# Kernel tuning notes

Hardware: AMD Instinct MI355X
Metric: run time of the kernel (lower is better)

## Reference

```python
import jax, jax.numpy as jnp
import numpy as np
from jax import lax

MAX_LEN = 50
MIN_LEN = 5
S = 2 * MAX_LEN + 1  # 101 states (2 branches)
NEG = -10000.0       # score for disallowed transitions


def _build_constraints():
    """Replicates CRFBaseModel.get_crf_constraints(max_len=50, min_len=5, n_branches=2)."""
    pairs = [(0, 0), (0, 1), (MAX_LEN, 1), (MAX_LEN, 0)]
    for i in range(1, MAX_LEN):
        pairs.append((i, i + 1))
        if i > MIN_LEN - 1:
            pairs.append((MIN_LEN - 2, i))
    pairs.append((MAX_LEN - 1, MAX_LEN))
    pairs.append((MAX_LEN - 1, MAX_LEN - 1))
    start_b = 1 + MAX_LEN
    end_b = 2 * MAX_LEN
    pairs += [(0, start_b), (end_b, start_b), (end_b, 0), (end_b, 1), (start_b - 1, start_b)]
    for i in range(start_b, end_b):
        pairs.append((i, i + 1))
        if i > MIN_LEN - 1:
            pairs.append((start_b + MIN_LEN - 3, i))
    pairs.append((end_b - 1, end_b - 1))
    allowed_t = np.zeros((S, S), dtype=bool)
    for (a, c) in pairs:
        allowed_t[a, c] = True
    allowed_s = np.zeros((S,), dtype=bool)
    allowed_s[[0, 1, start_b]] = True
    allowed_e = np.zeros((S,), dtype=bool)
    allowed_e[[0, MAX_LEN, end_b]] = True
    return allowed_t, allowed_s, allowed_e

_ALLOWED_T, _ALLOWED_S, _ALLOWED_E = _build_constraints()


def setup_inputs() -> dict:
    key = jax.random.key(0)
    k0, k1, k2, k3, k4 = jax.random.split(key, 5)
    B, T = 128, 2048
    features = jax.random.normal(k0, (B, T, 64), dtype=jnp.float32)
    mask = jnp.ones((B, T), dtype=bool)
    W = jax.random.normal(k1, (64, 3), dtype=jnp.float32) * 0.05
    b = jnp.zeros((3,), dtype=jnp.float32)
    start_transitions = jax.random.uniform(k2, (S,), minval=-0.1, maxval=0.1, dtype=jnp.float32)
    transitions = jax.random.uniform(k3, (S, S), minval=-0.1, maxval=0.1, dtype=jnp.float32)
    end_transitions = jax.random.uniform(k4, (S,), minval=-0.1, maxval=0.1, dtype=jnp.float32)
    return {"features": features, "mask": mask, "W": W, "b": b,
            "start_transitions": start_transitions, "transitions": transitions,
            "end_transitions": end_transitions}


def reference(features, mask, W, b, start_transitions, transitions, end_transitions):
    B, T, _ = features.shape
    # Apply hand-crafted transition constraints (disallowed -> -10000).
    trans = jnp.where(jnp.asarray(_ALLOWED_T), transitions, NEG)       # [S,S]
    start = jnp.where(jnp.asarray(_ALLOWED_S), start_transitions, NEG)  # [S]
    end = jnp.where(jnp.asarray(_ALLOWED_E), end_transitions, NEG)      # [S]

    # Emissions: linear head to 3 labels, repeated over the state space.
    e3 = features @ W + b  # [B,T,3]
    em = jnp.concatenate([
        e3[..., 0:1],
        jnp.broadcast_to(e3[..., 1:2], (B, T, MAX_LEN)),
        jnp.broadcast_to(e3[..., 2:3], (B, T, MAX_LEN)),
    ], axis=-1)  # [B,T,S]

    eT = jnp.moveaxis(em, 1, 0)    # [T,B,S]
    mT = jnp.moveaxis(mask, 1, 0)  # [T,B]

    # ---- forward (alpha) recursion ----
    a0 = start[None, :] + eT[0]  # [B,S]

    def fwd_step(a, inp):
        e_t, m_t = inp
        a_new = jax.nn.logsumexp(a[:, :, None] + trans[None], axis=1) + e_t
        a = jnp.where(m_t[:, None], a_new, a)
        return a, a

    _, alphas = lax.scan(fwd_step, a0, (eT[1:], mT[1:]))
    alpha = jnp.concatenate([a0[None], alphas], axis=0)  # [T,B,S]
    logZ = jax.nn.logsumexp(alpha[-1] + end[None, :], axis=-1)  # [B]

    # ---- backward (beta) recursion ----
    bT = jnp.broadcast_to(end[None, :], (B, S))

    def bwd_step(b_nxt, inp):
        e_nxt, m_nxt = inp
        b_new = jax.nn.logsumexp(trans[None] + (e_nxt + b_nxt)[:, None, :], axis=2)
        b_nxt = jnp.where(m_nxt[:, None], b_new, b_nxt)
        return b_nxt, b_nxt

    _, betas = lax.scan(bwd_step, bT, (eT[1:], mT[1:]), reverse=True)
    beta = jnp.concatenate([betas, bT[None]], axis=0)  # [T,B,S]

    # marginal probabilities p_t(s) = exp(alpha+beta-logZ) == softmax over states
    probs = jnp.moveaxis(jax.nn.softmax(alpha + beta, axis=-1), 0, 1)  # [B,T,S]

    # ---- Viterbi decode (top_k=1) ----
    def vit_step(v, inp):
        e_t, m_t = inp
        scores = v[:, :, None] + trans[None]   # [B,S_prev,S_cur]
        best = scores.max(axis=1)
        idx = scores.argmax(axis=1).astype(jnp.int32)
        v = jnp.where(m_t[:, None], best + e_t, v)
        return v, idx

    v_last, hist = lax.scan(vit_step, a0, (eT[1:], mT[1:]))  # hist: [T-1,B,S]
    final = v_last + end[None, :]
    last_state = jnp.argmax(final, axis=-1).astype(jnp.int32)  # [B]
    best_score = final.max(axis=-1)

    def back(state, h_t):
        prev = jnp.take_along_axis(h_t, state[:, None], axis=1)[:, 0]
        return prev, prev

    _, prevs = lax.scan(back, last_state, hist, reverse=True)  # [T-1,B]
    paths = jnp.concatenate([prevs, last_state[None]], axis=0).T  # [B,T]
    path_probs = jnp.exp(best_score - logZ)  # [B]
    return probs, paths, path_probs
```

## Files before the change

kernel.cpp:

```cpp
#include <hip/hip_runtime.h>
#include <hip/hip_bf16.h>
#include <math.h>

#define Tn 2048
#define Bn 128
#define Sn 101
#define HP 112
#define CL 128
#define NC (Tn / CL)
#define SEG 256
#define KSEG 8
#define SEGA 128
#define KA 16
#define WWA 64
#define WWARMV 512
#define NEGV -10000.0f
#define DIS  -3.0e38f
#define NINF2 -1.0e30f
#define L2E  1.442695041f

__device__ __forceinline__ int state_label(int s) { return (s == 0) ? 0 : ((s <= 50) ? 1 : 2); }

__device__ __forceinline__ float rl(float v, int lane) {
    return __int_as_float(__builtin_amdgcn_readlane(__float_as_int(v), lane));
}
__device__ __forceinline__ float slog2(float x) {
    return (x > 0.f) ? __log2f(x) : NINF2;
}

__device__ __forceinline__ float dpp_shr1(float x) {
    int xi = __float_as_int(x);
    return __int_as_float(__builtin_amdgcn_update_dpp(xi, xi, 0x138, 0xf, 0xf, false));
}
__device__ __forceinline__ float dpp_shl1(float x) {
    int xi = __float_as_int(x);
    return __int_as_float(__builtin_amdgcn_update_dpp(xi, xi, 0x130, 0xf, 0xf, false));
}
__device__ __forceinline__ float dpp_sum63(float x) {
    x += __int_as_float(__builtin_amdgcn_update_dpp(0, __float_as_int(x), 0x111, 0xf, 0xf, false));
    x += __int_as_float(__builtin_amdgcn_update_dpp(0, __float_as_int(x), 0x112, 0xf, 0xf, false));
    x += __int_as_float(__builtin_amdgcn_update_dpp(0, __float_as_int(x), 0x114, 0xf, 0xf, false));
    x += __int_as_float(__builtin_amdgcn_update_dpp(0, __float_as_int(x), 0x118, 0xf, 0xf, false));
    x += __int_as_float(__builtin_amdgcn_update_dpp(0, __float_as_int(x), 0x142, 0xf, 0xf, false));
    x += __int_as_float(__builtin_amdgcn_update_dpp(0, __float_as_int(x), 0x143, 0xf, 0xf, false));
    return x;
}
__device__ __forceinline__ float dpp_max63(float x) {
    x = fmaxf(x, __int_as_float(__builtin_amdgcn_update_dpp(0, __float_as_int(x), 0x111, 0xf, 0xf, false)));
    x = fmaxf(x, __int_as_float(__builtin_amdgcn_update_dpp(0, __float_as_int(x), 0x112, 0xf, 0xf, false)));
    x = fmaxf(x, __int_as_float(__builtin_amdgcn_update_dpp(0, __float_as_int(x), 0x114, 0xf, 0xf, false)));
    x = fmaxf(x, __int_as_float(__builtin_amdgcn_update_dpp(0, __float_as_int(x), 0x118, 0xf, 0xf, false)));
    x = fmaxf(x, __int_as_float(__builtin_amdgcn_update_dpp(0, __float_as_int(x), 0x142, 0xf, 0xf, false)));
    x = fmaxf(x, __int_as_float(__builtin_amdgcn_update_dpp(0, __float_as_int(x), 0x143, 0xf, 0xf, false)));
    return x;
}
__device__ __forceinline__ void renorm2(float& a, float& b, float& sh) {
    float m = rl(dpp_max63(fmaxf(a, b)), 63);
    int mi = __float_as_int(m);
    if (mi == 0) return;
    int e = ((mi >> 23) & 255) - 127;
    float sc = __int_as_float((127 - e) << 23);
    a *= sc; b *= sc; sh += (float)e;
}

__device__ __forceinline__ float lse2_tree(float vA, float vB) {
    float m = fmaxf(vA, vB);
    float z = exp2f(vA - m) + exp2f(vB - m);
    #pragma unroll
    for (int o = 32; o; o >>= 1) {
        float mo = __shfl_xor(m, o), zo = __shfl_xor(z, o);
        float mx = fmaxf(m, mo);
        z = z * exp2f(m - mx) + zo * exp2f(mo - mx);
        m = mx;
    }
    return m + __log2f(z);
}

__device__ __forceinline__ void load_panel(const float* __restrict__ e3, size_t ebase, int pb, int l,
                                           float& q0, float& q1, float& q2) {
    int tr = pb + l;
    if (tr > Tn - 1) tr = Tn - 1;
    if (tr < 0) tr = 0;
    const float* p = e3 + (ebase + tr) * 3;
    q0 = p[0]; q1 = p[1]; q2 = p[2];
}
__device__ __forceinline__ void panel_sel2(float q0, float q1, float q2, int u,
                                           int l, float& eA, float& eB) {
    float s0 = rl(q0, u), s1 = rl(q1, u), s2 = rl(q2, u);
    eA = (l == 0) ? s0 : ((l <= 25) ? s1 : s2);
    eB = (l <= 24) ? s1 : s2;
}

__device__ __forceinline__ void bwd_lin(float eA, float eB, float& bA, float& bB,
    float wAc, float wBc, float wAs, float wBs, float wA2, float wA3,
    float w3A, float w3B, float w53A, float w53B, int l)
{
    float yA = eA * bA, yB = eB * bB;
    float yAdn = dpp_shl1(yA);
    float y0 = rl(yA, 0), y1 = rl(yB, 0), y51 = rl(yB, 25);
    float c3 = w3A * yA + w3B * yB;
    float c53 = w53A * yA + w53B * yB;
    float s3 = rl(dpp_sum63(c3), 63);
    float s53 = rl(dpp_sum63(c53), 63);
    float chA = (l == 50) ? y51 : yB;
    float nA = wAc * chA + wAs * yA + wA2 * y0 + wA3 * ((l == 0) ? y51 : y1);
    float nB = wBc * yAdn + wBs * yB;
    nB = (l == 1) ? s3 : ((l == 26) ? s53 : nB);
    bA = nA; bB = nB;
}

__global__ __launch_bounds__(256) void k_emis(const float* __restrict__ feat,
                                              const float* __restrict__ W,
                                              const float* __restrict__ bb,
                                              float* __restrict__ e3) {
    int row = blockIdx.x * 256 + threadIdx.x;
    if (row >= Bn * Tn) return;
    const float* f = feat + (size_t)row * 64;
    double a0 = 0.0, a1 = 0.0, a2 = 0.0;
    for (int i = 0; i < 64; i++) {
        double fv = (double)f[i];
        a0 += fv * (double)W[i * 3 + 0];
        a1 += fv * (double)W[i * 3 + 1];
        a2 += fv * (double)W[i * 3 + 2];
    }
    e3[(size_t)row * 3 + 0] = (float)(a0 + (double)bb[0]);
    e3[(size_t)row * 3 + 1] = (float)(a1 + (double)bb[1]);
    e3[(size_t)row * 3 + 2] = (float)(a2 + (double)bb[2]);
}

__global__ __launch_bounds__(64) void kA(const float* __restrict__ e3,
                                         const float* __restrict__ trans,
                                         const float* __restrict__ startT,
                                         const float* __restrict__ endT,
                                         float* __restrict__ alphaOut,
                                         float* __restrict__ shf,
                                         float* __restrict__ wA,
                                         float* __restrict__ outLast,
                                         float* __restrict__ LSEend,
                                         float* __restrict__ bhand)
{
    const int bid = blockIdx.x;
    const int l = threadIdx.x;
    const int sA = 2 * l, sB = 2 * l + 1;
    const bool hA = sA <= 100, hB = sB <= 100;
    const int lblA = state_label(hA ? sA : 100);
    const int lblB = state_label(hB ? sB : 100);

    if (bid < 2048) {
        const int b = bid >> 4, j = bid & 15;
        const size_t ebase = (size_t)b * Tn;
        const int t0 = j * SEGA, t1 = t0 + SEGA;
        int ts = t0 - WWA; if (ts < 0) ts = 0;
        float trAc = (hA && sA >= 1) ? trans[(sA - 1) * Sn + sA] : DIS;
        float trBc = hB ? trans[(sB - 1) * Sn + sB] : DIS;
        float trA1 = (sA >= 5 && sA <= 49) ? trans[3 * Sn + sA] : ((hA && sA <= 1) ? trans[50 * Sn + sA] : DIS);
        float trB1 = (sB >= 5 && sB <= 49) ? trans[3 * Sn + sB] : ((hB && sB <= 1) ? trans[50 * Sn + sB] : DIS);
        float trA2 = ((sA == 51 || sA == 52) || (sA >= 55 && sA <= 99)) ? trans[53 * Sn + sA]
                   : ((hA && sA <= 1) ? trans[100 * Sn + sA] : DIS);
        float trB2 = ((sB == 51 || sB == 52) || (sB >= 55 && sB <= 99)) ? trans[53 * Sn + sB]
                   : ((hB && sB <= 1) ? trans[100 * Sn + sB] : DIS);
        float trA3 = (sA == 0) ? trans[0] : DIS;
        float trB3 = (sB == 49 || sB == 53 || sB == 99) ? trans[sB * Sn + sB] : ((sB == 51) ? trans[0 * Sn + 51] : DIS);
        float trBx = (sB == 51) ? trans[100 * Sn + 51] : DIS;
        float wAc = __expf(trAc), wB0 = __expf(trBc), wA1 = __expf(trA1), wB1 = __expf(trB1);
        float wA2w = __expf(trA2), wB2 = __expf(trB2), wA3w = __expf(trA3), wB3 = __expf(trB3), wBx = __expf(trBx);
        float scA = (sA == 0 || sA == 1 || sA == 51) ? startT[sA] : NEGV;
        float scB = (sB == 1 || sB == 51) ? startT[sB] : NEGV;
        float enA = (sA == 0 || sA == 50 || sA == 100) ? endT[sA] : NEGV;

        float p0, p1, p2, n0 = 0.f, n1 = 0.f, n2 = 0.f;
        int pb = ts + 1;
        load_panel(e3, ebase, pb, l, p0, p1, p2);
        p0 = __expf(p0); p1 = __expf(p1); p2 = __expf(p2);

        float aA, aB, sh = 0.f;
        if (ts == 0) {
            float e0A = e3[ebase * 3 + lblA], e0B = e3[ebase * 3 + lblB];
            aA = __expf(scA + e0A);
            aB = __expf(scB + e0B);
            if (j == 0) {
                size_t r = ebase * Sn;
                if (hA) alphaOut[r + sA] = aA;
                if (hB) alphaOut[r + sB] = aB;
                if (l == 0) shf[ebase] = 0.f;
            }
        } else { aA = 1.f; aB = 1.f; }
        int rn = 0;
        int tb = ts + 1;
        for (; tb + 8 <= t0; tb += 8) {
            if ((rn++ & 1) == 0) renorm2(aA, aB, sh);
            if (tb - pb >= 64) { p0 = __expf(n0); p1 = __expf(n1); p2 = __expf(n2); pb += 64; }
            if (tb - pb == 48 && pb + 64 < t1) load_panel(e3, ebase, pb + 64, l, n0, n1, n2);
            #pragma unroll
            for (int v = 0; v < 8; ++v) {
                int t = tb + v;
                float eA, eB;
                panel_sel2(p0, p1, p2, t - pb, l, eA, eB);
                float chA = dpp_shr1(aB);
                float h3 = rl(aB, 1), h53 = rl(aB, 26);
                float a0v = rl(aA, 0), a50v = rl(aA, 25), a100v = rl(aA, 50);
                float s1v = (l == 0) ? a50v : h3;
                float s2v = (l == 0) ? a100v : h53;
                float zA = wAc * chA + wA1 * s1v + wA2w * s2v + wA3w * aA;
                float zB = wB0 * aA + wB1 * s1v + wB2 * s2v + wB3 * ((l == 25) ? a0v : aB) + wBx * a100v;
                aA = zA * eA; aB = zB * eB;
            }
        }
        for (; tb < t1; tb += 8) {
            if ((rn++ & 1) == 0) renorm2(aA, aB, sh);
            if (tb - pb >= 64) { p0 = __expf(n0); p1 = __expf(n1); p2 = __expf(n2); pb += 64; }
            if (tb - pb == 48 && pb + 64 < t1) load_panel(e3, ebase, pb + 64, l, n0, n1, n2);
            #pragma unroll
            for (int v = 0; v < 8; ++v) {
                int t = tb + v;
                if (t < t1) {
                    float eA, eB;
                    panel_sel2(p0, p1, p2, t - pb, l, eA, eB);
                    float chA = dpp_shr1(aB);
                    float h3 = rl(aB, 1), h53 = rl(aB, 26);
                    float a0v = rl(aA, 0), a50v = rl(aA, 25), a100v = rl(aA, 50);
                    float s1v = (l == 0) ? a50v : h3;
                    float s2v = (l == 0) ? a100v : h53;
                    float zA = wAc * chA + wA1 * s1v + wA2w * s2v + wA3w * aA;
                    float zB = wB0 * aA + wB1 * s1v + wB2 * s2v + wB3 * ((l == 25) ? a0v : aB) + wBx * a100v;
                    aA = zA * eA; aB = zB * eB;
                    if (t >= t0) {
                        size_t r = (ebase + t) * Sn;
                        if (hA) alphaOut[r + sA] = aA;
                        if (hB) alphaOut[r + sB] = aB;
                        if (l == 0) shf[ebase + t] = sh;
                    }
                    if (t == t0 - 1 && l == 0) wA[b * KA + j] = slog2(aA) + sh;
                }
            }
        }
        if (l == 0) outLast[b * KA + j] = slog2(aA) + sh;
        if (j == KA - 1) {
            float N = lse2_tree(hA ? slog2(aA) + sh + enA * L2E : NINF2,
                                hB ? slog2(aB) + sh + NEGV * L2E : NINF2);
            if (l == 0) LSEend[b] = N;
        }
    } else {
        const int x = bid - 2048;
        const int b = x >> 4, j = x & 15;
        const size_t ebase = (size_t)b * Tn;
        const int tend = j * SEGA + SEGA;
        int te = tend + WWA; if (te > Tn - 1) te = Tn - 1;
        float trAc = (l < 50) ? trans[sA * Sn + sA + 1] : ((l == 50) ? trans[100 * Sn + 51] : DIS);
        float trBc = (hB && l != 1 && l != 26) ? trans[sB * Sn + sB + 1] : DIS;
        float trAs = (sA == 0) ? trans[0] : DIS;
        float trBs = (sB == 49) ? trans[49 * Sn + 49] : ((sB == 99) ? trans[99 * Sn + 99] : DIS);
        float trA2c = (sA == 50) ? trans[50 * Sn + 0] : ((sA == 100) ? trans[100 * Sn + 0] : DIS);
        float trA3c = (sA == 0) ? trans[0 * Sn + 51]
                    : ((sA == 50) ? trans[50 * Sn + 1] : ((sA == 100) ? trans[100 * Sn + 1] : DIS));
        float tr3A = (sA >= 4 && sA <= 49) ? trans[3 * Sn + sA] : DIS;
        float tr3B = (sB >= 4 && sB <= 49) ? trans[3 * Sn + sB] : DIS;
        float tr53A = (sA >= 51 && sA <= 99) ? trans[53 * Sn + sA] : DIS;
        float tr53B = (sB >= 51 && sB <= 99) ? trans[53 * Sn + sB] : DIS;
        float wAc = __expf(trAc), wBc = __expf(trBc), wAs = __expf(trAs), wBs = __expf(trBs);
        float wA2 = __expf(trA2c), wA3 = __expf(trA3c);
        float w3A = __expf(tr3A), w3B = __expf(tr3B), w53A = __expf(tr53A), w53B = __expf(tr53B);
        float bA, bB, sh = 0.f;
        if (te == Tn - 1) {
            bA = (sA == 0 || sA == 50 || sA == 100) ? __expf(endT[sA]) : 0.f;
            bB = 0.f;
        } else { bA = 1.f; bB = 1.f; }
        if (te > tend) {
            float p0, p1, p2, n0 = 0.f, n1 = 0.f, n2 = 0.f;
            int pb = te - 63;
            load_panel(e3, ebase, pb, l, p0, p1, p2);
            p0 = __expf(p0); p1 = __expf(p1); p2 = __expf(p2);
            int rn = 0;
            for (int tc = te; tc > tend; tc -= 8) {
                if ((rn++ & 1) == 0) renorm2(bA, bB, sh);
                if (tc < pb) { p0 = __expf(n0); p1 = __expf(n1); p2 = __expf(n2); pb -= 64; }
                if (tc - pb == 7 && pb - 1 > tend) load_panel(e3, ebase, pb - 64, l, n0, n1, n2);
                #pragma unroll
                for (int v = 0; v < 8; ++v) {
                    int tcur = tc - v;
                    if (tcur > tend) {
                        float eA, eB;
                        panel_sel2(p0, p1, p2, tcur - pb, l, eA, eB);
                        bwd_lin(eA, eB, bA, bB, wAc, wBc, wAs, wBs, wA2, wA3,
                                w3A, w3B, w53A, w53B, l);
                    }
                }
            }
        }
        float* h0 = bhand + (size_t)(b * KA + j) * 104;
        if (l <= 50) { h0[2 * l] = slog2(bA) + sh; h0[2 * l + 1] = slog2(bB) + sh; }
    }
}

__global__ __launch_bounds__(64) void kB(const float* __restrict__ e3,
                                         const float* __restrict__ trans,
                                         const float* __restrict__ startT,
                                         const float* __restrict__ endT,
                                         const float* __restrict__ bhand,
                                         const float* __restrict__ shf,
                                         float* __restrict__ probsIO,
                                         unsigned char* __restrict__ hist,
                                         float* __restrict__ vW,
                                         float* __restrict__ vOut,
                                         float* __restrict__ best,
                                         int* __restrict__ last)
{
    const int bid = blockIdx.x;
    const int l = threadIdx.x;
    const int sA = 2 * l, sB = 2 * l + 1;
    const bool hA = sA <= 100, hB = sB <= 100;
    const int lblA = state_label(hA ? sA : 100);
    const int lblB = state_label(hB ? sB : 100);

    if (bid < 1024) {
        __builtin_amdgcn_s_setprio(1);
        const int b = bid >> 3, j = bid & 7;
        const size_t ebase = (size_t)b * Tn;
        const int t0 = j * SEG, t1 = t0 + SEG;
        int ts = t0 - WWARMV; if (ts < 0) ts = 0;
        float trAc = (hA && sA >= 1) ? trans[(sA - 1) * Sn + sA] : DIS;
        float trBc = hB ? trans[(sB - 1) * Sn + sB] : DIS;
        float trA1 = (sA >= 5 && sA <= 49) ? trans[3 * Sn + sA] : ((hA && sA <= 1) ? trans[50 * Sn + sA] : DIS);
        float trB1 = (sB >= 5 && sB <= 49) ? trans[3 * Sn + sB] : ((hB && sB <= 1) ? trans[50 * Sn + sB] : DIS);
        float trA2 = ((sA == 51 || sA == 52) || (sA >= 55 && sA <= 99)) ? trans[53 * Sn + sA]
                   : ((hA && sA <= 1) ? trans[100 * Sn + sA] : DIS);
        float trB2 = ((sB == 51 || sB == 52) || (sB >= 55 && sB <= 99)) ? trans[53 * Sn + sB]
                   : ((hB && sB <= 1) ? trans[100 * Sn + sB] : DIS);
        float trA3 = (sA == 0) ? trans[0] : DIS;
        float trB3 = (sB == 49 || sB == 53 || sB == 99) ? trans[sB * Sn + sB] : ((sB == 51) ? trans[0 * Sn + 51] : DIS);
        float trBx = (sB == 51) ? trans[100 * Sn + 51] : DIS;
        float scA = (sA == 0 || sA == 1 || sA == 51) ? startT[sA] : NEGV;
        float scB = (sB == 1 || sB == 51) ? startT[sB] : NEGV;
        float enA = (sA == 0 || sA == 50 || sA == 100) ? endT[sA] : NEGV;
        const int idxA1 = (sA <= 1) ? 50 : 3, idxB1 = (sB <= 1) ? 50 : 3;
        const int idxA2 = (sA <= 1) ? 100 : 53, idxB2 = (sB <= 1) ? 100 : 53;
        const int idxB3 = (sB == 51) ? 0 : sB;

        float p0, p1, p2, n0 = 0.f, n1 = 0.f, n2 = 0.f;
        int pb = ts + 1;
        load_panel(e3, ebase, pb, l, p0, p1, p2);

        float vA, vB;
        if (ts == 0) {
            vA = scA + e3[ebase * 3 + lblA];
            vB = scB + e3[ebase * 3 + lblB];
        } else { vA = 0.f; vB = 0.f; }
        size_t hoff = (ebase + (size_t)(t0 > 0 ? t0 - 1 : 0)) * HP + 2 * l;
        int tb = ts + 1;
        for (; tb + 8 <= t0; tb += 8) {
            if (tb - pb >= 64) { p0 = n0; p1 = n1; p2 = n2; pb += 64; }
            if (tb - pb == 48 && pb + 64 < t1) load_panel(e3, ebase, pb + 64, l, n0, n1, n2);
            #pragma unroll
            for (int v = 0; v < 8; ++v) {
                int t = tb + v;
                float eA, eB;
                panel_sel2(p0, p1, p2, t - pb, l, eA, eB);
                float chA = dpp_shr1(vB);
                float h3 = rl(vB, 1), h53 = rl(vB, 26);
                float a0v = rl(vA, 0), a50v = rl(vA, 25), a100v = rl(vA, 50);
                float s1v = (l == 0) ? a50v : h3;
                float s2v = (l == 0) ? a100v : h53;
                float tA0 = chA + trAc, tA1 = s1v + trA1, tA2 = s2v + trA2, tA3 = vA + trA3;
                float tB0 = vA + trBc, tB1 = s1v + trB1, tB2 = s2v + trB2;
                float tB3 = ((l == 25) ? a0v : vB) + trB3;
                float tBx = a100v + trBx;
                float bvA = fmaxf(fmaxf(tA0, tA1), fmaxf(tA2, tA3));
                float bvB = fmaxf(fmaxf(fmaxf(tB0, tB1), fmaxf(tB2, tB3)), tBx);
                vA = bvA + eA;
                vB = bvB + eB;
            }
        }
        for (; tb < t1; tb += 8) {
            if (tb - pb >= 64) { p0 = n0; p1 = n1; p2 = n2; pb += 64; }
            if (tb - pb == 48 && pb + 64 < t1) load_panel(e3, ebase, pb + 64, l, n0, n1, n2);
            #pragma unroll
            for (int v = 0; v < 8; ++v) {
                int t = tb + v;
                if (t < t1) {
                    float eA, eB;
                    panel_sel2(p0, p1, p2, t - pb, l, eA, eB);
                    float chA = dpp_shr1(vB);
                    float h3 = rl(vB, 1), h53 = rl(vB, 26);
                    float a0v = rl(vA, 0), a50v = rl(vA, 25), a100v = rl(vA, 50);
                    float s1v = (l == 0) ? a50v : h3;
                    float s2v = (l == 0) ? a100v : h53;
                    float tA0 = chA + trAc, tA1 = s1v + trA1, tA2 = s2v + trA2, tA3 = vA + trA3;
                    float tB0 = vA + trBc, tB1 = s1v + trB1, tB2 = s2v + trB2;
                    float tB3 = ((l == 25) ? a0v : vB) + trB3;
                    float tBx = a100v + trBx;
                    float bvA = fmaxf(fmaxf(tA0, tA1), fmaxf(tA2, tA3));
                    int biA = min(min((tA0 == bvA) ? (sA - 1) : 127, (tA1 == bvA) ? idxA1 : 127),
                                  min((tA2 == bvA) ? idxA2 : 127, (tA3 == bvA) ? sA : 127));
                    float bvB = fmaxf(fmaxf(fmaxf(tB0, tB1), fmaxf(tB2, tB3)), tBx);
                    int biB = min(min((tB0 == bvB) ? (sB - 1) : 127, (tB1 == bvB) ? idxB1 : 127),
                              min(min((tB2 == bvB) ? idxB2 : 127, (tB3 == bvB) ? idxB3 : 127),
                                  (tBx == bvB) ? 100 : 127));
                    if (t == t0 - 1 && l == 0) vW[b * KSEG + j] = bvA + eA;
                    vA = bvA + eA;
                    vB = bvB + eB;
                    if (t >= t0 && l <= 50) {
                        *reinterpret_cast<unsigned short*>(hist + hoff) =
                            (unsigned short)((biA & 0xff) | ((biB & 0xff) << 8));
                        hoff += HP;
                    }
                }
            }
        }
        if (l == 0) vOut[b * KSEG + j] = vA;
        if (j == KSEG - 1) {
            float fvA = hA ? vA + enA : DIS;
            float fvB = DIS;
            float bv; int bi;
            if (fvA >= fvB) { bv = fvA; bi = sA; } else { bv = fvB; bi = sB; }
            #pragma unroll
            for (int o = 32; o; o >>= 1) {
                float ov = __shfl_xor(bv, o);
                int oi = __shfl_xor(bi, o);
                if (ov > bv || (ov == bv && oi < bi)) { bv = ov; bi = oi; }
            }
            if (l == 0) { best[b] = bv; last[b] = bi; }
        }
    } else {
        const int x = bid - 1024;
        const int b = x >> 4, j = x & 15;
        const size_t ebase = (size_t)b * Tn;
        const size_t base = ebase * Sn;
        const int tlo = j * SEGA;
        const int tstart = (j == KA - 1) ? (Tn - 1) : (tlo + SEGA);

        float trAc = (l < 50) ? trans[sA * Sn + sA + 1] : ((l == 50) ? trans[100 * Sn + 51] : DIS);
        float trBc = (hB && l != 1 && l != 26) ? trans[sB * Sn + sB + 1] : DIS;
        float trAs = (sA == 0) ? trans[0] : DIS;
        float trBs = (sB == 49) ? trans[49 * Sn + 49] : ((sB == 99) ? trans[99 * Sn + 99] : DIS);
        float trA2c = (sA == 50) ? trans[50 * Sn + 0] : ((sA == 100) ? trans[100 * Sn + 0] : DIS);
        float trA3c = (sA == 0) ? trans[0 * Sn + 51]
                    : ((sA == 50) ? trans[50 * Sn + 1] : ((sA == 100) ? trans[100 * Sn + 1] : DIS));
        float tr3A = (sA >= 4 && sA <= 49) ? trans[3 * Sn + sA] : DIS;
        float tr3B = (sB >= 4 && sB <= 49) ? trans[3 * Sn + sB] : DIS;
        float tr53A = (sA >= 51 && sA <= 99) ? trans[53 * Sn + sA] : DIS;
        float tr53B = (sB >= 51 && sB <= 99) ? trans[53 * Sn + sB] : DIS;
        float wAc = __expf(trAc), wBc = __expf(trBc), wAs = __expf(trAs), wBs = __expf(trBs);
        float wA2 = __expf(trA2c), wA3 = __expf(trA3c);
        float w3A = __expf(tr3A), w3B = __expf(tr3B), w53A = __expf(tr53A), w53B = __expf(tr53B);

        const float* hh = bhand + (size_t)(b * KA + j) * 104;
        float blA = (l <= 50) ? hh[2 * l] : NINF2;
        float blB = (l <= 50) ? hh[2 * l + 1] : NINF2;
        float m = fmaxf(blA, blB);
        #pragma unroll
        for (int o = 32; o; o >>= 1) m = fmaxf(m, __shfl_xor(m, o));
        float sh = m;
        float bA = exp2f(blA - m), bB = exp2f(blB - m);

        float p0, p1, p2, n0 = 0.f, n1 = 0.f, n2 = 0.f;
        int pb = tstart - 63;
        load_panel(e3, ebase, pb, l, p0, p1, p2);
        p0 = __expf(p0); p1 = __expf(p1); p2 = __expf(p2);

        float aRA[8], aRB[8], shR[8];
        #pragma unroll
        for (int u = 0; u < 8; ++u) {
            int ra = tstart - 1 - u; if (ra < 0) ra = 0;
            aRA[u] = probsIO[base + (size_t)ra * Sn + sA];
            aRB[u] = probsIO[base + (size_t)ra * Sn + sB];
            shR[u] = shf[ebase + ra];
        }
        float invS = 1.f, shA0 = 0.f, sh0 = 0.f;
        bool haveN = false;
        if (j == KA - 1) {
            float a0 = probsIO[base + (size_t)(Tn - 1) * Sn + sA];
            float a1 = probsIO[base + (size_t)(Tn - 1) * Sn + sB];
            float shAt = shf[ebase + Tn - 1];
            float prod = (hA ? a0 * bA : 0.f) + (hB ? a1 * bB : 0.f);
            float S = rl(dpp_sum63(prod), 63);
            invS = 1.f / S; shA0 = shAt; sh0 = sh; haveN = true;
            size_t r = base + (size_t)(Tn - 1) * Sn;
            float pA = a0 * bA * invS, pB = a1 * bB * invS;
            if (l < 50) { probsIO[r + sA] = pA; probsIO[r + sB] = pB; }
            else if (l == 50) probsIO[r + sA] = pA;
        }
        int rn = 0;
        for (int tc = tstart; tc > tlo; tc -= 8) {
            if ((rn++ & 1) == 0) renorm2(bA, bB, sh);
            if (tc < pb) { p0 = __expf(n0); p1 = __expf(n1); p2 = __expf(n2); pb -= 64; }
            if (tc - pb == 7 && pb - 1 > tlo) load_panel(e3, ebase, pb - 64, l, n0, n1, n2);
            #pragma unroll
            for (int u = 0; u < 8; ++u) {
                int tcur = tc - u;
                if (tcur > tlo) {
                    float eA, eB;
                    panel_sel2(p0, p1, p2, tcur - pb, l, eA, eB);
                    bwd_lin(eA, eB, bA, bB, wAc, wBc, wAs, wBs, wA2, wA3,
                            w3A, w3B, w53A, w53B, l);
                    float aA = aRA[u], aB = aRB[u];
                    float shAt = shR[u];
                    if (!haveN) {
                        float prod = (hA ? aA * bA : 0.f) + (hB ? aB * bB : 0.f);
                        float S = rl(dpp_sum63(prod), 63);
                        invS = 1.f / S; shA0 = shAt; sh0 = sh; haveN = true;
                    }
                    float scale = exp2f((shAt - shA0) + (sh - sh0)) * invS;
                    size_t r = base + (size_t)(tcur - 1) * Sn;
                    float pA = aA * bA * scale, pB = aB * bB * scale;
                    if (l < 50) { probsIO[r + sA] = pA; probsIO[r + sB] = pB; }
                    else if (l == 50) probsIO[r + sA] = pA;
                    int rnx = tcur - 9; if (rnx < 0) rnx = 0;
                    aRA[u] = probsIO[base + (size_t)rnx * Sn + sA];
                    aRB[u] = probsIO[base + (size_t)rnx * Sn + sB];
                    shR[u] = shf[ebase + rnx];
                }
            }
        }
    }
}

__global__ __launch_bounds__(64) void kC(const unsigned char* __restrict__ hist,
                                         unsigned char* __restrict__ M)
{
    __shared__ unsigned char lh[CL * HP];
    int blk = blockIdx.x; int b = blk >> 4; int c = blk & 15;
    if (c == 0) return;
    const int4* src = (const int4*)(hist + ((size_t)b * Tn + (c * CL - 1)) * HP);
    int4* dst = (int4*)lh;
    for (int i = threadIdx.x; i < CL * HP / 16; i += 64) dst[i] = src[i];
    __syncthreads();
    int cur0 = threadIdx.x;
    int cur1 = threadIdx.x + 64;
    bool h1v = cur1 < Sn;
    if (!h1v) cur1 = 0;
    for (int r = CL - 1; r >= 0; r--) {
        cur0 = lh[r * HP + cur0];
        cur1 = lh[r * HP + cur1];
    }
    M[((size_t)b * NC + c) * HP + threadIdx.x] = (unsigned char)cur0;
    if (h1v) M[((size_t)b * NC + c) * HP + threadIdx.x + 64] = (unsigned char)cur1;
}

__global__ __launch_bounds__(128) void kD(const unsigned char* __restrict__ hist,
                                          const unsigned char* __restrict__ Mmap,
                                          const int* __restrict__ last,
                                          const float* __restrict__ wA,
                                          const float* __restrict__ outLast,
                                          const float* __restrict__ LSEend,
                                          const float* __restrict__ vW,
                                          const float* __restrict__ vOut,
                                          const float* __restrict__ best,
                                          float* __restrict__ paths,
                                          float* __restrict__ pathp) {
    int blk = blockIdx.x; int b = blk >> 4; int c = blk & 15;
    __shared__ unsigned char lh[(CL - 1) * HP];
    __shared__ unsigned char pl[CL];
    const int4* src = (const int4*)(hist + ((size_t)b * Tn + c * CL) * HP);
    int4* dst = (int4*)lh;
    for (int i = threadIdx.x; i < (CL - 1) * HP / 16; i += 128) dst[i] = src[i];
    if (threadIdx.x == 1 && c == 0) {
        float cA = 0.f, cV = 0.f;
        for (int k = 1; k < KA; ++k) cA += wA[b * KA + k] - outLast[b * KA + k - 1];
        for (int k = 1; k < KSEG; ++k) cV += vOut[b * KSEG + k - 1] - vW[b * KSEG + k];
        float logZ2 = LSEend[b] - cA;
        float bestT = best[b] + cV;
        pathp[b] = exp2f(bestT * L2E - logZ2);
    }
    __syncthreads();
    if (threadIdx.x == 0) {
        int s = last[b];
        for (int cc = NC - 1; cc > c; cc--) s = (int)Mmap[((size_t)b * NC + cc) * HP + s];
        pl[CL - 1] = (unsigned char)s;
        for (int r = CL - 2; r >= 0; r--) { s = lh[r * HP + s]; pl[r] = (unsigned char)s; }
    }
    __syncthreads();
    paths[(size_t)b * Tn + c * CL + threadIdx.x] = (float)pl[threadIdx.x];
}

extern "C" void kernel_launch(void* const* d_in, const int* in_sizes, int n_in,
                              void* d_out, int out_size, void* d_ws, size_t ws_size,
                              hipStream_t stream) {
    const float* feat   = (const float*)d_in[0];
    const float* W      = (const float*)d_in[2];
    const float* bb     = (const float*)d_in[3];
    const float* startT = (const float*)d_in[4];
    const float* trans  = (const float*)d_in[5];
    const float* endT   = (const float*)d_in[6];

    float* out = (float*)d_out;
    float* probs = out;
    float* paths = out + (size_t)Bn * Tn * Sn;
    float* pathp = paths + (size_t)Bn * Tn;

    char* ws = (char*)d_ws;
    size_t off = 0;
    float* e3 = (float*)(ws + off);                    off += (size_t)Bn * Tn * 3 * sizeof(float);
    unsigned char* hist = (unsigned char*)(ws + off);  off += (size_t)Bn * Tn * HP;
    unsigned char* Mmap = (unsigned char*)(ws + off);  off += (size_t)Bn * NC * HP;
    off = (off + 15) & ~(size_t)15;
    float* shf     = (float*)(ws + off); off += (size_t)Bn * Tn * sizeof(float);
    float* wA      = (float*)(ws + off); off += Bn * KA * sizeof(float);
    float* outLast = (float*)(ws + off); off += Bn * KA * sizeof(float);
    float* LSEend  = (float*)(ws + off); off += Bn * sizeof(float);
    float* vW      = (float*)(ws + off); off += Bn * KSEG * sizeof(float);
    float* vOut    = (float*)(ws + off); off += Bn * KSEG * sizeof(float);
    float* best    = (float*)(ws + off); off += Bn * sizeof(float);
    int*   last    = (int*)(ws + off);   off += Bn * sizeof(int);
    off = (off + 15) & ~(size_t)15;
    float* bhand   = (float*)(ws + off); off += (size_t)Bn * KA * 104 * sizeof(float);

    k_emis<<<(Bn * Tn + 255) / 256, 256, 0, stream>>>(feat, W, bb, e3);
    kA<<<4096, 64, 0, stream>>>(e3, trans, startT, endT, probs, shf,
                                wA, outLast, LSEend, bhand);
    kB<<<3072, 64, 0, stream>>>(e3, trans, startT, endT, bhand, shf, probs, hist,
                                vW, vOut, best, last);
    kC<<<Bn * NC, 64, 0, stream>>>(hist, Mmap);
    kD<<<Bn * NC, 128, 0, stream>>>(hist, Mmap, last, wA, outLast, LSEend,
                                    vW, vOut, best, paths, pathp);
}
```

Before: 229.3 us.

## Run full-sequence Viterbi max-only scan to checkpoint segment starts, removing warmup recompute

Adds 128 high-priority blocks to the first kernel. Each runs a full-length max-plus Viterbi forward pass without argmax and writes exact score checkpoints every 256 steps, plus the best final score and last state. The segmented Viterbi kernel then starts each segment from its checkpoint instead of running a 512-step warmup, and the score-correction bookkeeping disappears. The cost is a long serial per-batch pass in the first kernel that may become its critical path.

New measurement: 331.9 us. 44.8% more time.

```diff
diff --git a/kernel.cpp b/kernel.cpp
--- a/kernel.cpp
+++ b/kernel.cpp
@@ -13,7 +13,6 @@
 #define SEGA 128
 #define KA 16
 #define WWA 64
-#define WWARMV 512
 #define NEGV -10000.0f
 #define DIS  -3.0e38f
 #define NINF2 -1.0e30f
@@ -128,7 +127,7 @@
     e3[(size_t)row * 3 + 2] = (float)(a2 + (double)bb[2]);
 }
 
-__global__ __launch_bounds__(64) void kA(const float* __restrict__ e3,
+__global__ __launch_bounds__(64) void k1(const float* __restrict__ e3,
                                          const float* __restrict__ trans,
                                          const float* __restrict__ startT,
                                          const float* __restrict__ endT,
@@ -137,6 +136,9 @@
                                          float* __restrict__ wA,
                                          float* __restrict__ outLast,
                                          float* __restrict__ LSEend,
+                                         float* __restrict__ vchk,
+                                         float* __restrict__ best,
+                                         int* __restrict__ last,
                                          float* __restrict__ bhand)
 {
     const int bid = blockIdx.x;
@@ -146,8 +148,73 @@
     const int lblA = state_label(hA ? sA : 100);
     const int lblB = state_label(hB ? sB : 100);
 
-    if (bid < 2048) {
-        const int b = bid >> 4, j = bid & 15;
+    if (bid < 128) {
+        __builtin_amdgcn_s_setprio(1);
+        const int b = bid;
+        const size_t ebase = (size_t)b * Tn;
+        float trAc = (hA && sA >= 1) ? trans[(sA - 1) * Sn + sA] : DIS;
+        float trBc = hB ? trans[(sB - 1) * Sn + sB] : DIS;
+        float trA1 = (sA >= 5 && sA <= 49) ? trans[3 * Sn + sA] : ((hA && sA <= 1) ? trans[50 * Sn + sA] : DIS);
+        float trB1 = (sB >= 5 && sB <= 49) ? trans[3 * Sn + sB] : ((hB && sB <= 1) ? trans[50 * Sn + sB] : DIS);
+        float trA2 = ((sA == 51 || sA == 52) || (sA >= 55 && sA <= 99)) ? trans[53 * Sn + sA]
+                   : ((hA && sA <= 1) ? trans[100 * Sn + sA] : DIS);
+        float trB2 = ((sB == 51 || sB == 52) || (sB >= 55 && sB <= 99)) ? trans[53 * Sn + sB]
+                   : ((hB && sB <= 1) ? trans[100 * Sn + sB] : DIS);
+        float trA3 = (sA == 0) ? trans[0] : DIS;
+        float trB3 = (sB == 49 || sB == 53 || sB == 99) ? trans[sB * Sn + sB] : ((sB == 51) ? trans[0 * Sn + 51] : DIS);
+        float trBx = (sB == 51) ? trans[100 * Sn + 51] : DIS;
+        float scA = (sA == 0 || sA == 1 || sA == 51) ? startT[sA] : NEGV;
+        float scB = (sB == 1 || sB == 51) ? startT[sB] : NEGV;
+        float enA = (sA == 0 || sA == 50 || sA == 100) ? endT[sA] : NEGV;
+
+        float p0, p1, p2, n0 = 0.f, n1 = 0.f, n2 = 0.f;
+        int pb = 1;
+        load_panel(e3, ebase, pb, l, p0, p1, p2);
+        float vA = scA + e3[ebase * 3 + lblA];
+        float vB = scB + e3[ebase * 3 + lblB];
+        for (int tb = 1; tb < Tn; tb += 8) {
+            if (tb - pb >= 64) { p0 = n0; p1 = n1; p2 = n2; pb += 64; }
+            if (tb - pb == 48 && pb + 64 < Tn) load_panel(e3, ebase, pb + 64, l, n0, n1, n2);
+            #pragma unroll
+            for (int v = 0; v < 8; ++v) {
+                int t = tb + v;
+                if (t < Tn) {
+                    float eA, eB;
+                    panel_sel2(p0, p1, p2, t - pb, l, eA, eB);
+                    float chA = dpp_shr1(vB);
+                    float h3 = rl(vB, 1), h53 = rl(vB, 26);
+                    float a0v = rl(vA, 0), a50v = rl(vA, 25), a100v = rl(vA, 50);
+                    float s1v = (l == 0) ? a50v : h3;
+                    float s2v = (l == 0) ? a100v : h53;
+                    float tA0 = chA + trAc, tA1 = s1v + trA1, tA2 = s2v + trA2, tA3 = vA + trA3;
+                    float tB0 = vA + trBc, tB1 = s1v + trB1, tB2 = s2v + trB2;
+                    float tB3 = ((l == 25) ? a0v : vB) + trB3;
+                    float tBx = a100v + trBx;
+                    float bvA = fmaxf(fmaxf(tA0, tA1), fmaxf(tA2, tA3));
+                    float bvB = fmaxf(fmaxf(fmaxf(tB0, tB1), fmaxf(tB2, tB3)), tBx);
+                    vA = bvA + eA;
+                    vB = bvB + eB;
+                    if ((t & 255) == 255 && t < 1792) {
+                        float* c = vchk + ((size_t)(b * 7 + (t >> 8))) * 104;
+                        if (l <= 50) { c[2 * l] = vA; c[2 * l + 1] = vB; }
+                    }
+                }
+            }
+        }
+        float fvA = hA ? vA + enA : DIS;
+        float fvB = DIS;
+        float bv; int bi;
+        if (fvA >= fvB) { bv = fvA; bi = sA; } else { bv = fvB; bi = sB; }
+        #pragma unroll
+        for (int o = 32; o; o >>= 1) {
+            float ov = __shfl_xor(bv, o);
+            int oi = __shfl_xor(bi, o);
+            if (ov > bv || (ov == bv && oi < bi)) { bv = ov; bi = oi; }
+        }
+        if (l == 0) { best[b] = bv; last[b] = bi; }
+    } else if (bid < 2176) {
+        const int x = bid - 128;
+        const int b = x >> 4, j = x & 15;
         const size_t ebase = (size_t)b * Tn;
         const int t0 = j * SEGA, t1 = t0 + SEGA;
         int ts = t0 - WWA; if (ts < 0) ts = 0;
@@ -241,7 +308,7 @@
             if (l == 0) LSEend[b] = N;
         }
     } else {
-        const int x = bid - 2048;
+        const int x = bid - 2176;
         const int b = x >> 4, j = x & 15;
         const size_t ebase = (size_t)b * Tn;
         const int tend = j * SEGA + SEGA;
@@ -292,18 +359,14 @@
     }
 }
 
-__global__ __launch_bounds__(64) void kB(const float* __restrict__ e3,
+__global__ __launch_bounds__(64) void k2(const float* __restrict__ e3,
                                          const float* __restrict__ trans,
                                          const float* __restrict__ startT,
-                                         const float* __restrict__ endT,
                                          const float* __restrict__ bhand,
                                          const float* __restrict__ shf,
+                                         const float* __restrict__ vchk,
                                          float* __restrict__ probsIO,
-                                         unsigned char* __restrict__ hist,
-                                         float* __restrict__ vW,
-                                         float* __restrict__ vOut,
-                                         float* __restrict__ best,
-                                         int* __restrict__ last)
+                                         unsigned char* __restrict__ hist)
 {
     const int bid = blockIdx.x;
     const int l = threadIdx.x;
@@ -317,7 +380,7 @@
         const int b = bid >> 3, j = bid & 7;
         const size_t ebase = (size_t)b * Tn;
         const int t0 = j * SEG, t1 = t0 + SEG;
-        int ts = t0 - WWARMV; if (ts < 0) ts = 0;
+        const int tstart = (j == 0) ? 1 : t0;
         float trAc = (hA && sA >= 1) ? trans[(sA - 1) * Sn + sA] : DIS;
         float trBc = hB ? trans[(sB - 1) * Sn + sB] : DIS;
         float trA1 = (sA >= 5 && sA <= 49) ? trans[3 * Sn + sA] : ((hA && sA <= 1) ? trans[50 * Sn + sA] : DIS);
@@ -329,48 +392,26 @@
         float trA3 = (sA == 0) ? trans[0] : DIS;
         float trB3 = (sB == 49 || sB == 53 || sB == 99) ? trans[sB * Sn + sB] : ((sB == 51) ? trans[0 * Sn + 51] : DIS);
         float trBx = (sB == 51) ? trans[100 * Sn + 51] : DIS;
-        float scA = (sA == 0 || sA == 1 || sA == 51) ? startT[sA] : NEGV;
-        float scB = (sB == 1 || sB == 51) ? startT[sB] : NEGV;
-        float enA = (sA == 0 || sA == 50 || sA == 100) ? endT[sA] : NEGV;
         const int idxA1 = (sA <= 1) ? 50 : 3, idxB1 = (sB <= 1) ? 50 : 3;
         const int idxA2 = (sA <= 1) ? 100 : 53, idxB2 = (sB <= 1) ? 100 : 53;
         const int idxB3 = (sB == 51) ? 0 : sB;
 
-        float p0, p1, p2, n0 = 0.f, n1 = 0.f, n2 = 0.f;
-        int pb = ts + 1;
-        load_panel(e3, ebase, pb, l, p0, p1, p2);
-
         float vA, vB;
-        if (ts == 0) {
+        if (j == 0) {
+            float scA = (sA == 0 || sA == 1 || sA == 51) ? startT[sA] : NEGV;
+            float scB = (sB == 1 || sB == 51) ? startT[sB] : NEGV;
             vA = scA + e3[ebase * 3 + lblA];
             vB = scB + e3[ebase * 3 + lblB];
-        } else { vA = 0.f; vB = 0.f; }
-        size_t hoff = (ebase + (size_t)(t0 > 0 ? t0 - 1 : 0)) * HP + 2 * l;
-        int tb = ts + 1;
-        for (; tb + 8 <= t0; tb += 8) {
-            if (tb - pb >= 64) { p0 = n0; p1 = n1; p2 = n2; pb += 64; }
-            if (tb - pb == 48 && pb + 64 < t1) load_panel(e3, ebase, pb + 64, l, n0, n1, n2);
-            #pragma unroll
-            for (int v = 0; v < 8; ++v) {
-                int t = tb + v;
-                float eA, eB;
-                panel_sel2(p0, p1, p2, t - pb, l, eA, eB);
-                float chA = dpp_shr1(vB);
-                float h3 = rl(vB, 1), h53 = rl(vB, 26);
-                float a0v = rl(vA, 0), a50v = rl(vA, 25), a100v = rl(vA, 50);
-                float s1v = (l == 0) ? a50v : h3;
-                float s2v = (l == 0) ? a100v : h53;
-                float tA0 = chA + trAc, tA1 = s1v + trA1, tA2 = s2v + trA2, tA3 = vA + trA3;
-                float tB0 = vA + trBc, tB1 = s1v + trB1, tB2 = s2v + trB2;
-                float tB3 = ((l == 25) ? a0v : vB) + trB3;
-                float tBx = a100v + trBx;
-                float bvA = fmaxf(fmaxf(tA0, tA1), fmaxf(tA2, tA3));
-                float bvB = fmaxf(fmaxf(fmaxf(tB0, tB1), fmaxf(tB2, tB3)), tBx);
-                vA = bvA + eA;
-                vB = bvB + eB;
-            }
-        }
-        for (; tb < t1; tb += 8) {
+        } else {
+            const float* c = vchk + ((size_t)(b * 7 + (j - 1))) * 104;
+            vA = (l <= 50) ? c[2 * l] : 0.f;
+            vB = (l <= 50) ? c[2 * l + 1] : 0.f;
+        }
+        float p0, p1, p2, n0 = 0.f, n1 = 0.f, n2 = 0.f;
+        int pb = tstart;
+        load_panel(e3, ebase, pb, l, p0, p1, p2);
+        size_t hoff = (ebase + (size_t)(tstart - 1)) * HP + 2 * l;
+        for (int tb = tstart; tb < t1; tb += 8) {
             if (tb - pb >= 64) { p0 = n0; p1 = n1; p2 = n2; pb += 64; }
             if (tb - pb == 48 && pb + 64 < t1) load_panel(e3, ebase, pb + 64, l, n0, n1, n2);
             #pragma unroll
@@ -395,30 +436,15 @@
                     int biB = min(min((tB0 == bvB) ? (sB - 1) : 127, (tB1 == bvB) ? idxB1 : 127),
                               min(min((tB2 == bvB) ? idxB2 : 127, (tB3 == bvB) ? idxB3 : 127),
                                   (tBx == bvB) ? 100 : 127));
-                    if (t == t0 - 1 && l == 0) vW[b * KSEG + j] = bvA + eA;
                     vA = bvA + eA;
                     vB = bvB + eB;
-                    if (t >= t0 && l <= 50) {
+                    if (l <= 50) {
                         *reinterpret_cast<unsigned short*>(hist + hoff) =
                             (unsigned short)((biA & 0xff) | ((biB & 0xff) << 8));
                         hoff += HP;
                     }
                 }
             }
-        }
-        if (l == 0) vOut[b * KSEG + j] = vA;
-        if (j == KSEG - 1) {
-            float fvA = hA ? vA + enA : DIS;
-            float fvB = DIS;
-            float bv; int bi;
-            if (fvA >= fvB) { bv = fvA; bi = sA; } else { bv = fvB; bi = sB; }
-            #pragma unroll
-            for (int o = 32; o; o >>= 1) {
-                float ov = __shfl_xor(bv, o);
-                int oi = __shfl_xor(bi, o);
-                if (ov > bv || (ov == bv && oi < bi)) { bv = ov; bi = oi; }
-            }
-            if (l == 0) { best[b] = bv; last[b] = bi; }
         }
     } else {
         const int x = bid - 1024;
@@ -542,8 +568,6 @@
                                           const float* __restrict__ wA,
                                           const float* __restrict__ outLast,
                                           const float* __restrict__ LSEend,
-                                          const float* __restrict__ vW,
-                                          const float* __restrict__ vOut,
                                           const float* __restrict__ best,
                                           float* __restrict__ paths,
                                           float* __restrict__ pathp) {
@@ -554,12 +578,10 @@
     int4* dst = (int4*)lh;
     for (int i = threadIdx.x; i < (CL - 1) * HP / 16; i += 128) dst[i] = src[i];
     if (threadIdx.x == 1 && c == 0) {
-        float cA = 0.f, cV = 0.f;
+        float cA = 0.f;
         for (int k = 1; k < KA; ++k) cA += wA[b * KA + k] - outLast[b * KA + k - 1];
-        for (int k = 1; k < KSEG; ++k) cV += vOut[b * KSEG + k - 1] - vW[b * KSEG + k];
         float logZ2 = LSEend[b] - cA;
-        float bestT = best[b] + cV;
-        pathp[b] = exp2f(bestT * L2E - logZ2);
+        pathp[b] = exp2f(best[b] * L2E - logZ2);
     }
     __syncthreads();
     if (threadIdx.x == 0) {
@@ -597,19 +619,17 @@
     float* wA      = (float*)(ws + off); off += Bn * KA * sizeof(float);
     float* outLast = (float*)(ws + off); off += Bn * KA * sizeof(float);
     float* LSEend  = (float*)(ws + off); off += Bn * sizeof(float);
-    float* vW      = (float*)(ws + off); off += Bn * KSEG * sizeof(float);
-    float* vOut    = (float*)(ws + off); off += Bn * KSEG * sizeof(float);
+    float* vchk    = (float*)(ws + off); off += (size_t)Bn * 7 * 104 * sizeof(float);
     float* best    = (float*)(ws + off); off += Bn * sizeof(float);
     int*   last    = (int*)(ws + off);   off += Bn * sizeof(int);
     off = (off + 15) & ~(size_t)15;
     float* bhand   = (float*)(ws + off); off += (size_t)Bn * KA * 104 * sizeof(float);
 
     k_emis<<<(Bn * Tn + 255) / 256, 256, 0, stream>>>(feat, W, bb, e3);
-    kA<<<4096, 64, 0, stream>>>(e3, trans, startT, endT, probs, shf,
-                                wA, outLast, LSEend, bhand);
-    kB<<<3072, 64, 0, stream>>>(e3, trans, startT, endT, bhand, shf, probs, hist,
-                                vW, vOut, best, last);
+    k1<<<4224, 64, 0, stream>>>(e3, trans, startT, endT, probs, shf,
+                                wA, outLast, LSEend, vchk, best, last, bhand);
+    k2<<<3072, 64, 0, stream>>>(e3, trans, startT, bhand, shf, vchk, probs, hist);
     kC<<<Bn * NC, 64, 0, stream>>>(hist, Mmap);
     kD<<<Bn * NC, 128, 0, stream>>>(hist, Mmap, last, wA, outLast, LSEend,
-                                    vW, vOut, best, paths, pathp);
-}
+                                    best, paths, pathp);
+}
```
